# Optimization experiments

Hardware: AMD Instinct MI355X
Metric: run time of the kernel (lower is better)

The kernel has to match this reference:

```python
import jax, jax.numpy as jnp
import numpy as np

E = 8   # num routed experts
K = 1   # top-k per token
D = 512   # embed_dim
I = 2048  # moe_inter_dim (= 4*D)
B, T = 2, 2048


def setup_inputs() -> dict:
    key = jax.random.key(0)
    ks = jax.random.split(key, 7)
    s = 0.02
    x = jax.random.normal(ks[0], (B, T, D), jnp.float32)
    gate_w = jax.random.normal(ks[1], (E, D), jnp.float32) * s      # TopKGate.proj.weight
    w1 = jax.random.normal(ks[2], (E, I, D), jnp.float32) * s       # Expert.w1.weight per expert
    w2 = jax.random.normal(ks[3], (E, D, I), jnp.float32) * s       # Expert.w2.weight
    w3 = jax.random.normal(ks[4], (E, I, D), jnp.float32) * s       # Expert.w3.weight
    sw1 = jax.random.normal(ks[5], (I, D), jnp.float32) * s         # shared Linear(dim -> 1*inter)
    sw2 = jax.random.normal(ks[6], (D, I), jnp.float32) * s         # shared Linear(inter -> dim)
    return {"x": x, "gate_w": gate_w, "w1": w1, "w2": w2, "w3": w3, "sw1": sw1, "sw2": sw2}


def reference(x, gate_w, w1, w2, w3, sw1, sw2):
    xf = x.reshape(-1, D)                                  # [N, D]
    # gate: logits -> topk -> softmax over selected logits
    logits = xf @ gate_w.T                                 # [N, E]
    wts, idx = jax.lax.top_k(logits, K)                    # [N, K]
    wts = jax.nn.softmax(wts, axis=-1)
    # per-token combine weight for each expert (0 if not routed) -- identical
    # math to the torch gather/scatter loop, fully vectorized over experts.
    comb = jnp.einsum('nke,nk->ne', jax.nn.one_hot(idx, E, dtype=xf.dtype), wts)  # [N, E]
    # SwiGLU experts, batched over the expert axis
    h = jax.nn.silu(jnp.einsum('nd,eid->nei', xf, w1)) * jnp.einsum('nd,eid->nei', xf, w3)  # [N, E, I]
    y = jnp.einsum('nei,edi->nd', h * comb[:, :, None], w2)  # weighted combine
    # shared expert: Linear -> GELU(exact) -> Linear
    y = y + jax.nn.gelu(xf @ sw1.T, approximate=False) @ sw2.T
    return y.reshape(x.shape)
```

## Files before the change

### kernel.cpp

```cpp
#include <hip/hip_runtime.h>
#include <hip/hip_bf16.h>
#include <math.h>

#define N_TOK 4096
#define DIM 512
#define IDIM 2048
#define NEXP 8

#define W1_ELS 8388608
#define W3_ELS 8388608
#define W2_ELS 8388608
#define SW1_ELS 1048576
#define SW2_ELS 1048576
#define CONV_ELS 27262976
#define CONV_CHUNKS 3407872

typedef __attribute__((ext_vector_type(8))) short bf16x8;
typedef __attribute__((ext_vector_type(4))) float floatx4;

__device__ __forceinline__ short f2bf(float f) {
  unsigned int u;
  __builtin_memcpy(&u, &f, 4);
  u += 0x7fff + ((u >> 16) & 1);
  return (short)(u >> 16);
}

__device__ __forceinline__ bf16x8 ld8f(const float* __restrict__ p) {
  float4 a = *(const float4*)p;
  float4 b = *(const float4*)(p + 4);
  bf16x8 v;
  v[0] = f2bf(a.x); v[1] = f2bf(a.y); v[2] = f2bf(a.z); v[3] = f2bf(a.w);
  v[4] = f2bf(b.x); v[5] = f2bf(b.y); v[6] = f2bf(b.z); v[7] = f2bf(b.w);
  return v;
}

__device__ __forceinline__ float gelu_exactish(float v) {
  float z = fabsf(v) * 0.70710678118f;
  float tt = 1.f / (1.f + 0.3275911f * z);
  float poly = tt * (0.254829592f + tt * (-0.284496736f + tt * (1.421413741f +
               tt * (-1.453152027f + tt * 1.061405429f))));
  float er = 1.f - poly * __expf(-z * z);
  er = (v < 0.f) ? -er : er;
  return 0.5f * v * (1.f + er);
}

__device__ __forceinline__ void gll(const short* g, short* l) {
  __builtin_amdgcn_global_load_lds(
      (const __attribute__((address_space(1))) void*)g,
      (__attribute__((address_space(3))) void*)l, 16, 0, 0);
}

__global__ __launch_bounds__(256) void gate_conv_kernel(
    const float* __restrict__ x, const float* __restrict__ gw,
    short* __restrict__ xb, int* __restrict__ expert_id,
    const float* __restrict__ w1, const float* __restrict__ w3,
    const float* __restrict__ w2, const float* __restrict__ sw1,
    const float* __restrict__ sw2,
    short* __restrict__ w1b, short* __restrict__ w3b, short* __restrict__ w2b,
    short* __restrict__ sw1b, short* __restrict__ sw2b) {
  __shared__ float xs[16 * 516];
  __shared__ double ps[16][8][2];
  int t = threadIdx.x;

  if (blockIdx.x >= 256) {
    long nconv = (long)(gridDim.x - 256) * 256;
    long tidg = (long)(blockIdx.x - 256) * 256 + t;
    for (long c = tidg; c < CONV_CHUNKS; c += nconv) {
      long i = c * 8;
      const float* src;
      short* dst;
      long off;
      if (i < W1_ELS)                          { src = w1;  dst = w1b;  off = i; }
      else if (i < 2L * W1_ELS)                { src = w3;  dst = w3b;  off = i - W1_ELS; }
      else if (i < 3L * W1_ELS)                { src = w2;  dst = w2b;  off = i - 2L * W1_ELS; }
      else if (i < 3L * W1_ELS + SW1_ELS)      { src = sw1; dst = sw1b; off = i - 3L * W1_ELS; }
      else                                     { src = sw2; dst = sw2b; off = i - 3L * W1_ELS - SW1_ELS; }
      *(bf16x8*)(dst + off) = ld8f(src + off);
    }
    return;
  }

  int tok0 = blockIdx.x * 16;
  const float* xrow = x + (long)tok0 * DIM;
  for (int i = t; i < 2048; i += 256) {
    float4 v = ((const float4*)xrow)[i];
    int row = i >> 7, c4 = i & 127;
    *(float4*)&xs[row * 516 + c4 * 4] = v;
    short4 b;
    b.x = f2bf(v.x); b.y = f2bf(v.y); b.z = f2bf(v.z); b.w = f2bf(v.w);
    *(short4*)(xb + (long)tok0 * DIM + i * 4) = b;
  }
  __syncthreads();
  int tok = t & 15, e = (t >> 4) & 7, hf = t >> 7;
  const float* xr = &xs[tok * 516 + hf * 256];
  const float* wr = gw + e * DIM + hf * 256;
  double s = 0.0;
  for (int k = 0; k < 256; k += 4) {
    float4 xv = *(const float4*)(xr + k);
    float4 wv = *(const float4*)(wr + k);
    s += (double)xv.x * wv.x + (double)xv.y * wv.y +
         (double)xv.z * wv.z + (double)xv.w * wv.w;
  }
  ps[tok][e][hf] = s;
  __syncthreads();
  if (t < 16) {
    double best = ps[t][0][0] + ps[t][0][1];
    int bi = 0;
#pragma unroll
    for (int j = 1; j < 8; j++) {
      double v = ps[t][j][0] + ps[t][j][1];
      if (v > best) { best = v; bi = j; }
    }
    expert_id[tok0 + t] = bi;
  }
}

__global__ __launch_bounds__(256) void scan_scatter(
    const int* __restrict__ expert_id, int* __restrict__ counts,
    int* __restrict__ offsets, int* __restrict__ cursors, int* __restrict__ nmeta,
    int* __restrict__ te1, int* __restrict__ tr1,
    int* __restrict__ te2, int* __restrict__ tr2, int* __restrict__ perm) {
  __shared__ int cnt[8];
  int tid = threadIdx.x;
  if (tid < 8) cnt[tid] = 0;
  __syncthreads();
  for (int t = tid; t < N_TOK; t += 256) atomicAdd(&cnt[expert_id[t]], 1);
  __syncthreads();
  if (tid == 0) {
    int acc = 0;
    for (int e = 0; e < NEXP; e++) {
      counts[e] = cnt[e];
      offsets[e] = acc;
      cursors[e] = acc;
      acc += cnt[e];
    }
    int n1 = 0;
    for (int e = 0; e < NEXP; e++)
      for (int r = 0; r < cnt[e]; r += 128) { te1[n1] = e; tr1[n1] = r; n1++; }
    for (int r = 0; r < N_TOK; r += 128) { te1[n1] = 8; tr1[n1] = r; n1++; }
    int n2 = 0;
    for (int e = 0; e < NEXP; e++)
      for (int r = 0; r < cnt[e]; r += 64) { te2[n2] = e; tr2[n2] = r; n2++; }
    nmeta[0] = n1;
    nmeta[1] = n2;
  }
  __syncthreads();
  for (int t = tid; t < N_TOK; t += 256) {
    int e = expert_id[t];
    int slot = atomicAdd(&cursors[e], 1);
    perm[slot] = t;
  }
}

__global__ __launch_bounds__(256, 4) void stage1(
    const short* __restrict__ xb, const short* __restrict__ w1b,
    const short* __restrict__ w3b, const short* __restrict__ sw1b,
    short* __restrict__ h, short* __restrict__ g,
    const int* __restrict__ counts, const int* __restrict__ offsets,
    const int* __restrict__ nmeta, const int* __restrict__ te,
    const int* __restrict__ tr, const int* __restrict__ perm) {
  __shared__ short Al[128 * 64];
  __shared__ short B1l[64 * 64];
  __shared__ short B2l[64 * 64];
  int t = blockIdx.y;
  if (t >= nmeta[0]) return;
  int e = te[t], row0 = tr[t];
  bool routed = (e < 8);
  int cnt = routed ? counts[e] : N_TOK;
  int base = routed ? offsets[e] : 0;
  int n0 = blockIdx.x * 64;
  int tid = threadIdx.x, lane = tid & 63, w = tid >> 6;
  int wm = w >> 1, wn = w & 1;
  const short* B1 = routed ? w1b + (long)e * IDIM * DIM : sw1b;
  const short* B2 = w3b + (long)e * IDIM * DIM;

  int aoff[4], lbA[4];
#pragma unroll
  for (int j = 0; j < 4; j++) {
    int c = w * 256 + j * 64 + lane;
    int row = c >> 3, klog = (c & 7) ^ (row & 7);
    int srow = row0 + row;
    int slot = base + ((srow < cnt) ? srow : (cnt - 1));
    aoff[j] = perm[slot] * DIM + klog * 8;
    lbA[j] = (w * 256 + j * 64) * 8;
  }
  int bgoff[2], lbB[2];
#pragma unroll
  for (int i = 0; i < 2; i++) {
    int c = i * 256 + tid;
    int row = c >> 3, klog = (c & 7) ^ (row & 7);
    bgoff[i] = (n0 + row) * DIM + klog * 8;
    lbB[i] = (i * 256 + w * 64) * 8;
  }

  floatx4 acc[2][4][2];
#pragma unroll
  for (int m = 0; m < 2; m++)
#pragma unroll
    for (int i = 0; i < 4; i++)
#pragma unroll
      for (int j = 0; j < 2; j++) acc[m][i][j] = (floatx4)0.f;

  for (int kc = 0; kc < DIM; kc += 64) {
#pragma unroll
    for (int j = 0; j < 4; j++) gll(xb + aoff[j] + kc, &Al[lbA[j]]);
#pragma unroll
    for (int i = 0; i < 2; i++) gll(B1 + bgoff[i] + kc, &B1l[lbB[i]]);
    if (routed) {
#pragma unroll
      for (int i = 0; i < 2; i++) gll(B2 + bgoff[i] + kc, &B2l[lbB[i]]);
    }
    __syncthreads();

#pragma unroll
    for (int kf = 0; kf < 2; kf++) {
      int kp = (kf * 4 + (lane >> 4)) ^ (lane & 7);
      bf16x8 af[4];
#pragma unroll
      for (int mf = 0; mf < 4; mf++) {
        int row = wm * 64 + mf * 16 + (lane & 15);
        af[mf] = *(const bf16x8*)&Al[row * 64 + kp * 8];
      }
#pragma unroll
      for (int nf = 0; nf < 2; nf++) {
        int col = wn * 32 + nf * 16 + (lane & 15);
        bf16x8 b1 = *(const bf16x8*)&B1l[col * 64 + kp * 8];
#pragma unroll
        for (int mf = 0; mf < 4; mf++)
          acc[0][mf][nf] = __builtin_amdgcn_mfma_f32_16x16x32_bf16(
              af[mf], b1, acc[0][mf][nf], 0, 0, 0);
        if (routed) {
          bf16x8 b2 = *(const bf16x8*)&B2l[col * 64 + kp * 8];
#pragma unroll
          for (int mf = 0; mf < 4; mf++)
            acc[1][mf][nf] = __builtin_amdgcn_mfma_f32_16x16x32_bf16(
                af[mf], b2, acc[1][mf][nf], 0, 0, 0);
        }
      }
    }
    __syncthreads();
  }

  int quad = lane >> 4;
  int colb = n0 + wn * 32 + (lane & 15);
  short* dst = routed ? h : g;
#pragma unroll
  for (int mf = 0; mf < 4; mf++)
#pragma unroll
    for (int r = 0; r < 4; r++) {
      int srow = row0 + wm * 64 + mf * 16 + quad * 4 + r;
      if (srow >= cnt) continue;
      long ro = (long)(base + srow) * IDIM + colb;
      if (routed) {
#pragma unroll
        for (int nf = 0; nf < 2; nf++) {
          float a1 = acc[0][mf][nf][r];
          float a3 = acc[1][mf][nf][r];
          dst[ro + nf * 16] = f2bf((a1 / (1.f + __expf(-a1))) * a3);
        }
      } else {
#pragma unroll
        for (int nf = 0; nf < 2; nf++)
          dst[ro + nf * 16] = f2bf(gelu_exactish(acc[0][mf][nf][r]));
      }
    }
}

__global__ __launch_bounds__(256, 8) void stage2(
    const short* __restrict__ h, const short* __restrict__ g,
    const short* __restrict__ w2b, const short* __restrict__ sw2b,
    float* __restrict__ out, const int* __restrict__ counts,
    const int* __restrict__ offsets, const int* __restrict__ nmeta,
    const int* __restrict__ te, const int* __restrict__ tr,
    const int* __restrict__ perm) {
  __shared__ short Al[64 * 64];
  __shared__ short Bl[64 * 64];
  int t = blockIdx.y;
  if (t >= nmeta[1]) return;
  int e = te[t], row0 = tr[t];
  int cnt = counts[e], base = offsets[e];
  const short* w2e = w2b + (long)e * DIM * IDIM;
  int n0 = blockIdx.x * 64;
  int tid = threadIdx.x, lane = tid & 63, w = tid >> 6;
  int wm = w >> 1, wn = w & 1;

  int aoff[2], lbA[2], bgoff[2], lbB[2];
#pragma unroll
  for (int i = 0; i < 2; i++) {
    int c = i * 256 + tid;
    int row = c >> 3, klog = (c & 7) ^ (row & 7);
    int srow = row0 + row;
    int arow = base + ((srow < cnt) ? srow : (cnt - 1));
    aoff[i] = arow * IDIM + klog * 8;
    lbA[i] = (i * 256 + w * 64) * 8;
    bgoff[i] = (n0 + row) * IDIM + klog * 8;
    lbB[i] = (i * 256 + w * 64) * 8;
  }

  floatx4 acc[2][2];
#pragma unroll
  for (int i = 0; i < 2; i++)
#pragma unroll
    for (int j = 0; j < 2; j++) acc[i][j] = (floatx4)0.f;

#pragma unroll
  for (int ph = 0; ph < 2; ph++) {
    const short* As = ph ? g : h;
    const short* Bs = ph ? sw2b : w2e;
    for (int kc = 0; kc < IDIM; kc += 64) {
#pragma unroll
      for (int i = 0; i < 2; i++) gll(As + aoff[i] + kc, &Al[lbA[i]]);
#pragma unroll
      for (int i = 0; i < 2; i++) gll(Bs + bgoff[i] + kc, &Bl[lbB[i]]);
      __syncthreads();

#pragma unroll
      for (int kf = 0; kf < 2; kf++) {
        int kp = (kf * 4 + (lane >> 4)) ^ (lane & 7);
        bf16x8 af[2];
#pragma unroll
        for (int mf = 0; mf < 2; mf++) {
          int row = wm * 32 + mf * 16 + (lane & 15);
          af[mf] = *(const bf16x8*)&Al[row * 64 + kp * 8];
        }
#pragma unroll
        for (int nf = 0; nf < 2; nf++) {
          int col = wn * 32 + nf * 16 + (lane & 15);
          bf16x8 bv = *(const bf16x8*)&Bl[col * 64 + kp * 8];
#pragma unroll
          for (int mf = 0; mf < 2; mf++)
            acc[mf][nf] = __builtin_amdgcn_mfma_f32_16x16x32_bf16(
                af[mf], bv, acc[mf][nf], 0, 0, 0);
        }
      }
      __syncthreads();
    }
  }

  int quad = lane >> 4;
  int colb = n0 + wn * 32 + (lane & 15);
#pragma unroll
  for (int mf = 0; mf < 2; mf++)
#pragma unroll
    for (int r = 0; r < 4; r++) {
      int srow = row0 + wm * 32 + mf * 16 + quad * 4 + r;
      if (srow >= cnt) continue;
      long ro = (long)perm[base + srow] * DIM + colb;
#pragma unroll
      for (int nf = 0; nf < 2; nf++) out[ro + nf * 16] = acc[mf][nf][r];
    }
}

extern "C" void kernel_launch(void* const* d_in, const int* in_sizes, int n_in,
                              void* d_out, int out_size, void* d_ws, size_t ws_size,
                              hipStream_t stream) {
  const float* x = (const float*)d_in[0];
  const float* gate_w = (const float*)d_in[1];
  const float* w1 = (const float*)d_in[2];
  const float* w2 = (const float*)d_in[3];
  const float* w3 = (const float*)d_in[4];
  const float* sw1 = (const float*)d_in[5];
  const float* sw2 = (const float*)d_in[6];
  float* out = (float*)d_out;

  char* ws = (char*)d_ws;
  int* counts = (int*)ws;
  int* offsets = counts + 8;
  int* cursors = offsets + 8;
  int* nmeta = cursors + 8;
  int* te1 = nmeta + 8;
  int* tr1 = te1 + 128;
  int* te2 = tr1 + 128;
  int* tr2 = te2 + 128;
  int* expert_id = tr2 + 128;
  int* perm = expert_id + N_TOK;
  short* xb = (short*)(ws + 65536);
  short* h = xb + (size_t)N_TOK * DIM;
  short* g = h + (size_t)N_TOK * IDIM;
  short* w1b = g + (size_t)N_TOK * IDIM;
  short* w3b = w1b + (size_t)W1_ELS;
  short* w2b = w3b + (size_t)W3_ELS;
  short* sw1b = w2b + (size_t)W2_ELS;
  short* sw2b = sw1b + (size_t)SW1_ELS;

  gate_conv_kernel<<<256 + 2048, 256, 0, stream>>>(
      x, gate_w, xb, expert_id, w1, w3, w2, sw1, sw2,
      w1b, w3b, w2b, sw1b, sw2b);
  scan_scatter<<<1, 256, 0, stream>>>(expert_id, counts, offsets, cursors, nmeta,
                                      te1, tr1, te2, tr2, perm);
  stage1<<<dim3(IDIM / 64, 72), 256, 0, stream>>>(
      xb, w1b, w3b, sw1b, h, g, counts, offsets, nmeta, te1, tr1, perm);
  stage2<<<dim3(DIM / 64, 72), 256, 0, stream>>>(
      h, g, w2b, sw2b, out, counts, offsets, nmeta, te2, tr2, perm);
}
```

Before: 280.0 us.

## Split stage2 K across routed/shared halves with atomics; coalesce stage1 stores via LDS

Stage2 now runs the routed-expert and shared-expert down-projections as separate blocks (grid z=2) and accumulates them into the output with float atomicAdd. The output is zeroed by extra blocks in the first kernel. Block indices are remapped so blocks sharing an expert tile spread across XCDs. Stage1 stages its bf16 epilogue through swizzled LDS so it can write 16-byte coalesced rows, and its occupancy hint is raised from 4 to 5. The aim is to double stage2 parallelism and cut scattered 2-byte stores, at the cost of atomic traffic and an extra output-zeroing pass.

Result: slower. 364.6 us (+30.2%).

```diff
diff --git a/kernel.cpp b/kernel.cpp
--- a/kernel.cpp
+++ b/kernel.cpp
@@ -14,6 +14,10 @@
 #define SW2_ELS 1048576
 #define CONV_ELS 27262976
 #define CONV_CHUNKS 3407872
+#define GATE_BLOCKS 256
+#define CONV_BLOCKS 2048
+#define ZERO_BLOCKS 32
+#define CONV_THREADS (CONV_BLOCKS * 256)
 
 typedef __attribute__((ext_vector_type(8))) short bf16x8;
 typedef __attribute__((ext_vector_type(4))) float floatx4;
@@ -57,15 +61,22 @@
     const float* __restrict__ w2, const float* __restrict__ sw1,
     const float* __restrict__ sw2,
     short* __restrict__ w1b, short* __restrict__ w3b, short* __restrict__ w2b,
-    short* __restrict__ sw1b, short* __restrict__ sw2b) {
+    short* __restrict__ sw1b, short* __restrict__ sw2b,
+    float* __restrict__ out) {
   __shared__ float xs[16 * 516];
   __shared__ double ps[16][8][2];
   int t = threadIdx.x;
 
-  if (blockIdx.x >= 256) {
-    long nconv = (long)(gridDim.x - 256) * 256;
-    long tidg = (long)(blockIdx.x - 256) * 256 + t;
-    for (long c = tidg; c < CONV_CHUNKS; c += nconv) {
+  if (blockIdx.x >= GATE_BLOCKS + CONV_BLOCKS) {
+    float4 z4 = {0.f, 0.f, 0.f, 0.f};
+    long i0 = (long)(blockIdx.x - GATE_BLOCKS - CONV_BLOCKS) * 256 + t;
+    for (long i = i0; i < (long)N_TOK * DIM / 4; i += (long)ZERO_BLOCKS * 256)
+      ((float4*)out)[i] = z4;
+    return;
+  }
+  if (blockIdx.x >= GATE_BLOCKS) {
+    long tidg = (long)(blockIdx.x - GATE_BLOCKS) * 256 + t;
+    for (long c = tidg; c < CONV_CHUNKS; c += CONV_THREADS) {
       long i = c * 8;
       const float* src;
       short* dst;
@@ -152,7 +163,7 @@
   }
 }
 
-__global__ __launch_bounds__(256, 4) void stage1(
+__global__ __launch_bounds__(256, 5) void stage1(
     const short* __restrict__ xb, const short* __restrict__ w1b,
     const short* __restrict__ w3b, const short* __restrict__ sw1b,
     short* __restrict__ h, short* __restrict__ g,
@@ -241,29 +252,44 @@
     __syncthreads();
   }
 
+  short* S = Al;
   int quad = lane >> 4;
-  int colb = n0 + wn * 32 + (lane & 15);
   short* dst = routed ? h : g;
 #pragma unroll
   for (int mf = 0; mf < 4; mf++)
 #pragma unroll
     for (int r = 0; r < 4; r++) {
-      int srow = row0 + wm * 64 + mf * 16 + quad * 4 + r;
-      if (srow >= cnt) continue;
-      long ro = (long)(base + srow) * IDIM + colb;
-      if (routed) {
-#pragma unroll
-        for (int nf = 0; nf < 2; nf++) {
-          float a1 = acc[0][mf][nf][r];
+      int lr = wm * 64 + mf * 16 + quad * 4 + r;
+      int sw = ((lr >> 2) & 3) << 4;
+#pragma unroll
+      for (int nf = 0; nf < 2; nf++) {
+        int lc = wn * 32 + nf * 16 + (lane & 15);
+        float a1 = acc[0][mf][nf][r];
+        short v;
+        if (routed) {
           float a3 = acc[1][mf][nf][r];
-          dst[ro + nf * 16] = f2bf((a1 / (1.f + __expf(-a1))) * a3);
+          v = f2bf((a1 / (1.f + __expf(-a1))) * a3);
+        } else {
+          v = f2bf(gelu_exactish(a1));
         }
-      } else {
-#pragma unroll
-        for (int nf = 0; nf < 2; nf++)
-          dst[ro + nf * 16] = f2bf(gelu_exactish(acc[0][mf][nf][r]));
+        S[lr * 64 + ((lc & 48) ^ sw) + (lc & 15)] = v;
       }
     }
+  __syncthreads();
+#pragma unroll
+  for (int pass = 0; pass < 2; pass++) {
+    int lr = pass * 64 + (tid >> 2);
+    int srow = row0 + lr;
+    if (srow < cnt) {
+      int p = (tid & 3) * 16;
+      int lcs = p ^ (((lr >> 2) & 3) << 4);
+      bf16x8 v0 = *(const bf16x8*)&S[lr * 64 + lcs];
+      bf16x8 v1 = *(const bf16x8*)&S[lr * 64 + lcs + 8];
+      long ro = (long)(base + srow) * IDIM + n0 + p;
+      *(bf16x8*)&dst[ro] = v0;
+      *(bf16x8*)&dst[ro + 8] = v1;
+    }
+  }
 }
 
 __global__ __launch_bounds__(256, 8) void stage2(
@@ -275,12 +301,17 @@
     const int* __restrict__ perm) {
   __shared__ short Al[64 * 64];
   __shared__ short Bl[64 * 64];
-  int t = blockIdx.y;
+  int lid = blockIdx.x + 8 * (blockIdx.y + 72 * blockIdx.z);
+  int logical = (lid & 7) * 144 + (lid >> 3);
+  int z = logical / 576;
+  int rem = logical - z * 576;
+  int t = rem >> 3;
+  int n0 = (rem & 7) * 64;
   if (t >= nmeta[1]) return;
   int e = te[t], row0 = tr[t];
   int cnt = counts[e], base = offsets[e];
-  const short* w2e = w2b + (long)e * DIM * IDIM;
-  int n0 = blockIdx.x * 64;
+  const short* As = z ? g : h;
+  const short* Bs = z ? sw2b : (w2b + (long)e * DIM * IDIM);
   int tid = threadIdx.x, lane = tid & 63, w = tid >> 6;
   int wm = w >> 1, wn = w & 1;
 
@@ -303,38 +334,33 @@
 #pragma unroll
     for (int j = 0; j < 2; j++) acc[i][j] = (floatx4)0.f;
 
-#pragma unroll
-  for (int ph = 0; ph < 2; ph++) {
-    const short* As = ph ? g : h;
-    const short* Bs = ph ? sw2b : w2e;
-    for (int kc = 0; kc < IDIM; kc += 64) {
-#pragma unroll
-      for (int i = 0; i < 2; i++) gll(As + aoff[i] + kc, &Al[lbA[i]]);
-#pragma unroll
-      for (int i = 0; i < 2; i++) gll(Bs + bgoff[i] + kc, &Bl[lbB[i]]);
-      __syncthreads();
-
-#pragma unroll
-      for (int kf = 0; kf < 2; kf++) {
-        int kp = (kf * 4 + (lane >> 4)) ^ (lane & 7);
-        bf16x8 af[2];
-#pragma unroll
-        for (int mf = 0; mf < 2; mf++) {
-          int row = wm * 32 + mf * 16 + (lane & 15);
-          af[mf] = *(const bf16x8*)&Al[row * 64 + kp * 8];
-        }
-#pragma unroll
-        for (int nf = 0; nf < 2; nf++) {
-          int col = wn * 32 + nf * 16 + (lane & 15);
-          bf16x8 bv = *(const bf16x8*)&Bl[col * 64 + kp * 8];
-#pragma unroll
-          for (int mf = 0; mf < 2; mf++)
-            acc[mf][nf] = __builtin_amdgcn_mfma_f32_16x16x32_bf16(
-                af[mf], bv, acc[mf][nf], 0, 0, 0);
-        }
+  for (int kc = 0; kc < IDIM; kc += 64) {
+#pragma unroll
+    for (int i = 0; i < 2; i++) gll(As + aoff[i] + kc, &Al[lbA[i]]);
+#pragma unroll
+    for (int i = 0; i < 2; i++) gll(Bs + bgoff[i] + kc, &Bl[lbB[i]]);
+    __syncthreads();
+
+#pragma unroll
+    for (int kf = 0; kf < 2; kf++) {
+      int kp = (kf * 4 + (lane >> 4)) ^ (lane & 7);
+      bf16x8 af[2];
+#pragma unroll
+      for (int mf = 0; mf < 2; mf++) {
+        int row = wm * 32 + mf * 16 + (lane & 15);
+        af[mf] = *(const bf16x8*)&Al[row * 64 + kp * 8];
       }
-      __syncthreads();
-    }
+#pragma unroll
+      for (int nf = 0; nf < 2; nf++) {
+        int col = wn * 32 + nf * 16 + (lane & 15);
+        bf16x8 bv = *(const bf16x8*)&Bl[col * 64 + kp * 8];
+#pragma unroll
+        for (int mf = 0; mf < 2; mf++)
+          acc[mf][nf] = __builtin_amdgcn_mfma_f32_16x16x32_bf16(
+              af[mf], bv, acc[mf][nf], 0, 0, 0);
+      }
+    }
+    __syncthreads();
   }
 
   int quad = lane >> 4;
@@ -347,7 +373,8 @@
       if (srow >= cnt) continue;
       long ro = (long)perm[base + srow] * DIM + colb;
 #pragma unroll
-      for (int nf = 0; nf < 2; nf++) out[ro + nf * 16] = acc[mf][nf][r];
+      for (int nf = 0; nf < 2; nf++)
+        atomicAdd(&out[ro + nf * 16], acc[mf][nf][r]);
     }
 }
 
@@ -383,13 +410,13 @@
   short* sw1b = w2b + (size_t)W2_ELS;
   short* sw2b = sw1b + (size_t)SW1_ELS;
 
-  gate_conv_kernel<<<256 + 2048, 256, 0, stream>>>(
+  gate_conv_kernel<<<GATE_BLOCKS + CONV_BLOCKS + ZERO_BLOCKS, 256, 0, stream>>>(
       x, gate_w, xb, expert_id, w1, w3, w2, sw1, sw2,
-      w1b, w3b, w2b, sw1b, sw2b);
+      w1b, w3b, w2b, sw1b, sw2b, out);
   scan_scatter<<<1, 256, 0, stream>>>(expert_id, counts, offsets, cursors, nmeta,
                                       te1, tr1, te2, tr2, perm);
   stage1<<<dim3(IDIM / 64, 72), 256, 0, stream>>>(
       xb, w1b, w3b, sw1b, h, g, counts, offsets, nmeta, te1, tr1, perm);
-  stage2<<<dim3(DIM / 64, 72), 256, 0, stream>>>(
+  stage2<<<dim3(DIM / 64, 72, 2), 256, 0, stream>>>(
       h, g, w2b, sw2b, out, counts, offsets, nmeta, te2, tr2, perm);
 }
```
